# Optimization experiments

Measured on AMD Instinct MI355X. Metric: run time of the kernel, lower is better.

Reference implementation:

```python
import jax, jax.numpy as jnp
import numpy as np

INPUT_DIM = 28
HIDDEN = 256
N_LAYERS = 4
OUT_DIM = 21


def setup_inputs() -> dict:
    key = jax.random.key(0)
    ks = jax.random.split(key, 20)
    s = 1.0 / np.sqrt(HIDDEN)  # PyTorch LSTM init scale
    x = jax.random.normal(ks[0], (256, 512, INPUT_DIM), dtype=jnp.float32)
    W_ih0 = jax.random.uniform(ks[1], (4 * HIDDEN, INPUT_DIM), minval=-s, maxval=s, dtype=jnp.float32)
    W_ih_rest = jax.random.uniform(ks[2], (N_LAYERS - 1, 4 * HIDDEN, HIDDEN), minval=-s, maxval=s, dtype=jnp.float32)
    W_hh = jax.random.uniform(ks[3], (N_LAYERS, 4 * HIDDEN, HIDDEN), minval=-s, maxval=s, dtype=jnp.float32)
    b_ih = jax.random.uniform(ks[4], (N_LAYERS, 4 * HIDDEN), minval=-s, maxval=s, dtype=jnp.float32)
    b_hh = jax.random.uniform(ks[5], (N_LAYERS, 4 * HIDDEN), minval=-s, maxval=s, dtype=jnp.float32)
    W_out = jax.random.uniform(ks[6], (OUT_DIM, HIDDEN), minval=-s, maxval=s, dtype=jnp.float32)
    b_out = jax.random.uniform(ks[7], (OUT_DIM,), minval=-s, maxval=s, dtype=jnp.float32)
    return {"x": x, "W_ih0": W_ih0, "W_ih_rest": W_ih_rest, "W_hh": W_hh,
            "b_ih": b_ih, "b_hh": b_hh, "W_out": W_out, "b_out": b_out}


def _lstm_layer(x, W_ih, W_hh, b_ih, b_hh):
    # x: [B, T, D_in] -> [B, T, H]. PyTorch gate order: i, f, g, o.
    B, T, _ = x.shape
    H = W_hh.shape[1]
    # Precompute input projections for all timesteps: [T, B, 4H]
    xp = jnp.einsum('btd,gd->tbg', x, W_ih) + b_ih + b_hh

    def step(carry, xt):
        h, c = carry
        gates = xt + h @ W_hh.T  # [B, 4H]
        i, f, g, o = jnp.split(gates, 4, axis=-1)
        i = jax.nn.sigmoid(i)
        f = jax.nn.sigmoid(f)
        g = jnp.tanh(g)
        o = jax.nn.sigmoid(o)
        c = f * c + i * g
        h = o * jnp.tanh(c)
        return (h, c), h

    h0 = jnp.zeros((B, H), dtype=x.dtype)
    c0 = jnp.zeros((B, H), dtype=x.dtype)
    _, hs = jax.lax.scan(step, (h0, c0), xp)  # hs: [T, B, H]
    return jnp.transpose(hs, (1, 0, 2))  # [B, T, H]


def reference(x, W_ih0, W_ih_rest, W_hh, b_ih, b_hh, W_out, b_out):
    h = _lstm_layer(x, W_ih0, W_hh[0], b_ih[0], b_hh[0])
    for l in range(1, N_LAYERS):
        h = _lstm_layer(h, W_ih_rest[l - 1], W_hh[l], b_ih[l], b_hh[l])
    last = h[:, -1, :]  # [B, H]
    return jax.nn.sigmoid(last @ W_out.T + b_out)  # [B, OUT_DIM]
```

## Files before the change

kernel.cpp:

```cpp
#include <hip/hip_runtime.h>
#include <stdint.h>


#define B 256
#define T 512
#define H 256
#define DIN 28
#define NWG 256
#define OUTD 21

typedef __attribute__((ext_vector_type(8))) __bf16 bf16x8;
typedef __attribute__((ext_vector_type(4))) float f32x4;
typedef __attribute__((ext_vector_type(4))) unsigned short u16x4;
typedef unsigned long long u64;

#define WS_FLAGS 0ull
#define WS_HBUF  65536ull
#define WS_H3F   (WS_HBUF + 4ull*4*B*H*2)
#define WS_XBF   (WS_H3F + (u64)B*H*4)
#define WS_WIH0  (WS_XBF + (u64)B*T*32*2)
#define WS_WIHR  (WS_WIH0 + 1024ull*32*2)
#define WS_WHHR  (WS_WIHR + 3ull*1024*256*2)
#define WS_BIAS  (WS_WHHR + 4ull*1024*256*2)
#define WS_ZERO  WS_XBF

__device__ __forceinline__ unsigned short f2bf(float f) {
  unsigned u = __builtin_bit_cast(unsigned, f);
  u += 0x7fffu + ((u >> 16) & 1u);
  return (unsigned short)(u >> 16);
}
__device__ __forceinline__ float sigf(float x) { return 1.f / (1.f + __expf(-x)); }
__device__ __forceinline__ float tanhfast(float x) {
  float e = __expf(2.f * x);
  return 1.f - 2.f / (e + 1.f);
}
__device__ __forceinline__ bf16x8 ldb8(const void* p) { return *(const bf16x8*)p; }

__device__ __forceinline__ void stg_coh8(void* p, u64 v) {
  __hip_atomic_store((u64*)p, v, __ATOMIC_RELAXED, __HIP_MEMORY_SCOPE_AGENT);
}
__device__ __forceinline__ u64 ldq(const u64* p) {
  return __hip_atomic_load(p, __ATOMIC_RELAXED, __HIP_MEMORY_SCOPE_AGENT);
}
__device__ __forceinline__ unsigned ldflag(const unsigned* f) {
  return __hip_atomic_load(f, __ATOMIC_RELAXED, __HIP_MEMORY_SCOPE_AGENT);
}

__global__ void prep_x(const float* __restrict__ x, unsigned short* __restrict__ xbf) {
  int tot = B * T * 32;
  for (int idx = blockIdx.x * blockDim.x + threadIdx.x; idx < tot;
       idx += gridDim.x * blockDim.x) {
    int kk = idx & 31;
    int bt = idx >> 5;
    float v = (kk < DIN) ? x[(size_t)bt * DIN + kk] : 0.f;
    xbf[idx] = f2bf(v);
  }
}

__global__ void prep_w(const float* __restrict__ wih0, const float* __restrict__ wihrest,
                       const float* __restrict__ whh, const float* __restrict__ bih,
                       const float* __restrict__ bhh,
                       unsigned short* __restrict__ wih0r, unsigned short* __restrict__ wihr,
                       unsigned short* __restrict__ whhr, float* __restrict__ biasr) {
  const int R0 = 1024 * 32, R1 = 3 * 1024 * 256, R2 = 4 * 1024 * 256, R3 = 4 * 1024;
  int tot = R0 + R1 + R2 + R3;
  for (int idx = blockIdx.x * blockDim.x + threadIdx.x; idx < tot;
       idx += gridDim.x * blockDim.x) {
    if (idx < R0) {
      int k = idx & 31, np = idx >> 5, g = np & 3, j = np >> 2;
      wih0r[idx] = f2bf(k < DIN ? wih0[(size_t)(g * 256 + j) * DIN + k] : 0.f);
    } else if (idx < R0 + R1) {
      int i = idx - R0;
      int k = i & 255, r = i >> 8, np = r & 1023, l = r >> 10, g = np & 3, j = np >> 2;
      wihr[i] = f2bf(wihrest[((size_t)l * 1024 + g * 256 + j) * 256 + k]);
    } else if (idx < R0 + R1 + R2) {
      int i = idx - R0 - R1;
      int k = i & 255, r = i >> 8, np = r & 1023, l = r >> 10, g = np & 3, j = np >> 2;
      whhr[i] = f2bf(whh[((size_t)l * 1024 + g * 256 + j) * 256 + k]);
    } else {
      int i = idx - R0 - R1 - R2;
      int np = i & 1023, l = i >> 10, g = np & 3, j = np >> 2;
      biasr[i] = bih[l * 1024 + g * 256 + j] + bhh[l * 1024 + g * 256 + j];
    }
  }
}

__device__ __forceinline__ bf16x8 lds_frag(const unsigned char* base, int row, int kb) {
  return *(const bf16x8*)(base + row * 1024 + (kb ^ ((row & 15) << 4)));
}

__device__ __forceinline__ void mstep(const unsigned char* Ast, const unsigned char* Ws,
                                      int kb, int ar0, int ar1, int br0, int br1,
                                      f32x4& a00, f32x4& a01, f32x4& a10, f32x4& a11) {
  bf16x8 a0 = lds_frag(Ast, ar0, kb);
  bf16x8 a1 = lds_frag(Ast, ar1, kb);
  bf16x8 b0 = lds_frag(Ws, br0, kb);
  bf16x8 b1 = lds_frag(Ws, br1, kb);
  a00 = __builtin_amdgcn_mfma_f32_16x16x32_bf16(a0, b0, a00, 0, 0, 0);
  a01 = __builtin_amdgcn_mfma_f32_16x16x32_bf16(a0, b1, a01, 0, 0, 0);
  a10 = __builtin_amdgcn_mfma_f32_16x16x32_bf16(a1, b0, a10, 0, 0, 0);
  a11 = __builtin_amdgcn_mfma_f32_16x16x32_bf16(a1, b1, a11, 0, 0, 0);
}

__launch_bounds__(256, 1)
__global__ void lstm_main(const unsigned short* __restrict__ xbf,
                          const unsigned short* __restrict__ wih0r,
                          const unsigned short* __restrict__ wihr,
                          const unsigned short* __restrict__ whhr,
                          const float* __restrict__ biasr,
                          const float* __restrict__ Wout, const float* __restrict__ bout,
                          unsigned short* __restrict__ hbuf, float* __restrict__ h3f,
                          unsigned* __restrict__ flags, float* __restrict__ out) {
  __shared__ unsigned char Ws[64 * 1024];
  __shared__ unsigned char Ast[64 * 1024];
  __shared__ float gates[64 * 68];

  const int tid = threadIdx.x;
  const int lane = tid & 63;
  const int w = tid >> 6;
  const int wb = w >> 1, wn = w & 1;
  const int bid = blockIdx.x;
  const int layer = (bid & 7) >> 1;
  const int wgl = ((bid >> 3) << 1) | (bid & 1);
  const int b0g = wgl >> 4;
  const int b0 = b0g * 64;
  const int ntile = wgl & 15;
  const int n0 = ntile * 64;
  const int j0 = ntile * 16;
  const int mygrp = layer * 4 + b0g;

  const int ngr = (layer == 0) ? 36 : 64;
  for (int i = tid; i < 64 * ngr; i += 256) {
    int row = i / ngr, blk = i % ngr;
    uint4 v;
    if (layer == 0) {
      if (blk < 4) v = *(const uint4*)(wih0r + (size_t)(n0 + row) * 32 + blk * 8);
      else v = *(const uint4*)(whhr + (size_t)(n0 + row) * 256 + (blk - 4) * 8);
    } else {
      if (blk < 32)
        v = *(const uint4*)(wihr + ((size_t)(layer - 1) * 1024 + n0 + row) * 256 + blk * 8);
      else
        v = *(const uint4*)(whhr + ((size_t)layer * 1024 + n0 + row) * 256 + (blk - 32) * 8);
    }
    *(uint4*)(Ws + row * 1024 + ((blk * 16) ^ ((row & 15) << 4))) = v;
  }
  const float bv0 = biasr[layer * 1024 + n0 + wn * 32 + (lane & 15)];
  const float bv1 = biasr[layer * 1024 + n0 + wn * 32 + 16 + (lane & 15)];
  __syncthreads();

  const int arow0 = wb * 32 + (lane & 15);
  const int arow1 = arow0 + 16;
  const int akoff2 = (lane >> 4) * 16;
  const int brow0 = wn * 32 + (lane & 15);
  const int brow1 = brow0 + 16;

  const int stg_blk = tid & 63;
  const int stg_r0 = tid >> 6;

  f32x4 creg = {0.f, 0.f, 0.f, 0.f};

  for (int t = 0; t < T; ++t) {
    if (tid == 0) {
      const unsigned* frec = (t > 0) ? &flags[mygrp * 512 + (t - 1)] : nullptr;
      const unsigned* fprev = (layer > 0) ? &flags[(mygrp - 4) * 512 + t] : nullptr;
      const unsigned* fdown = (layer < 3 && t >= 4) ? &flags[(mygrp + 4) * 512 + (t - 4)] : nullptr;
      for (;;) {
        unsigned a = frec ? ldflag(frec) : 16u;
        unsigned b = fprev ? ldflag(fprev) : 16u;
        unsigned c = fdown ? ldflag(fdown) : 16u;
        if (a >= 16u && b >= 16u && c >= 16u) break;
        __builtin_amdgcn_s_sleep(1);
      }
    }
    __syncthreads();
    asm volatile("" ::: "memory");

    const unsigned short* hbR = hbuf + ((size_t)layer * 4 + ((t + 3) & 3)) * 65536;
    if (layer == 0) {
      u64 qa[16], qb[16];
#pragma unroll
      for (int it = 0; it < 16; ++it) {
        int row = b0 + stg_r0 + it * 4;
        if (stg_blk < 4) {
          bf16x8 v = ldb8(xbf + ((size_t)row * T + t) * 32 + stg_blk * 8);
          qa[it] = ((const u64*)&v)[0];
          qb[it] = ((const u64*)&v)[1];
        } else if (stg_blk < 36) {
          const u64* s = (const u64*)(hbR + (size_t)row * 256 + (stg_blk - 4) * 8);
          qa[it] = ldq(s);
          qb[it] = ldq(s + 1);
        }
      }
      __builtin_amdgcn_sched_barrier(0);
      if (stg_blk < 36) {
#pragma unroll
        for (int it = 0; it < 16; ++it) {
          int row = stg_r0 + it * 4;
          uint4 v;
          ((u64*)&v)[0] = qa[it];
          ((u64*)&v)[1] = qb[it];
          *(uint4*)(Ast + row * 1024 + ((stg_blk * 16) ^ ((row & 15) << 4))) = v;
        }
      }
    } else {
      const unsigned short* hbP = hbuf + ((size_t)(layer - 1) * 4 + (t & 3)) * 65536;
      const unsigned short* src = (stg_blk < 32) ? hbP + stg_blk * 8 : hbR + (stg_blk - 32) * 8;
      u64 qa[16], qb[16];
#pragma unroll
      for (int it = 0; it < 16; ++it) {
        int row = b0 + stg_r0 + it * 4;
        const u64* s = (const u64*)(src + (size_t)row * 256);
        qa[it] = ldq(s);
        qb[it] = ldq(s + 1);
      }
      __builtin_amdgcn_sched_barrier(0);
#pragma unroll
      for (int it = 0; it < 16; ++it) {
        int row = stg_r0 + it * 4;
        uint4 v;
        ((u64*)&v)[0] = qa[it];
        ((u64*)&v)[1] = qb[it];
        *(uint4*)(Ast + row * 1024 + ((stg_blk * 16) ^ ((row & 15) << 4))) = v;
      }
    }
    __syncthreads();

    f32x4 a00 = {bv0, bv0, bv0, bv0};
    f32x4 a01 = {bv1, bv1, bv1, bv1};
    f32x4 a10 = a00, a11 = a01;
    if (layer == 0) {
#pragma unroll
      for (int ki = 0; ki < 9; ++ki)
        mstep(Ast, Ws, ki * 64 + akoff2, arow0, arow1, brow0, brow1, a00, a01, a10, a11);
    } else {
#pragma unroll
      for (int ki = 0; ki < 16; ++ki)
        mstep(Ast, Ws, ki * 64 + akoff2, arow0, arow1, brow0, brow1, a00, a01, a10, a11);
    }

    {
      int c = lane & 15, Rg = lane >> 4;
      *(f32x4*)&gates[(wn * 32 + c) * 68 + wb * 32 + Rg * 4] = a00;
      *(f32x4*)&gates[(wn * 32 + 16 + c) * 68 + wb * 32 + Rg * 4] = a01;
      *(f32x4*)&gates[(wn * 32 + c) * 68 + wb * 32 + 16 + Rg * 4] = a10;
      *(f32x4*)&gates[(wn * 32 + 16 + c) * 68 + wb * 32 + 16 + Rg * 4] = a11;
    }
    __syncthreads();

    {
      int brel = tid & 63, jq = tid >> 6;
      int b = b0 + brel;
      int jb = j0 + jq * 4;
      f32x4 cnew;
      float hv[4];
#pragma unroll
      for (int i2 = 0; i2 < 4; ++i2) {
        int jr = jq * 4 + i2;
        float ip = gates[(4 * jr + 0) * 68 + brel];
        float fp = gates[(4 * jr + 1) * 68 + brel];
        float gp = gates[(4 * jr + 2) * 68 + brel];
        float op = gates[(4 * jr + 3) * 68 + brel];
        float ii = sigf(ip), ff = sigf(fp), gg = tanhfast(gp), oo = sigf(op);
        float cc = ff * creg[i2] + ii * gg;
        cnew[i2] = cc;
        hv[i2] = oo * tanhfast(cc);
      }
      creg = cnew;
      u16x4 h4 = {f2bf(hv[0]), f2bf(hv[1]), f2bf(hv[2]), f2bf(hv[3])};
      stg_coh8(hbuf + ((size_t)layer * 4 + (t & 3)) * 65536 + (size_t)b * H + jb,
               __builtin_bit_cast(u64, h4));
      if (layer == 3 && t == T - 1) {
        float2 p01 = make_float2(hv[0], hv[1]);
        float2 p23 = make_float2(hv[2], hv[3]);
        stg_coh8(h3f + (size_t)b * H + jb, __builtin_bit_cast(u64, p01));
        stg_coh8(h3f + (size_t)b * H + jb + 2, __builtin_bit_cast(u64, p23));
      }
    }
    asm volatile("s_waitcnt vmcnt(0)" ::: "memory");
    __syncthreads();
    if (tid == 0)
      __hip_atomic_fetch_add(&flags[mygrp * 512 + t], 1u, __ATOMIC_RELAXED,
                             __HIP_MEMORY_SCOPE_AGENT);
  }

  if (layer == 3) {
    if (tid == 0) {
      while (ldflag(&flags[mygrp * 512 + (T - 1)]) < 16u) __builtin_amdgcn_s_sleep(1);
    }
    __syncthreads();
    asm volatile("" ::: "memory");
    for (int i = tid; i < 4 * 128; i += 256) {
      int bi = i >> 7, jj = (i & 127) * 2;
      u64 q = ldq((const u64*)(h3f + (size_t)(b0 + ntile * 4 + bi) * H + jj));
      float2 hf = __builtin_bit_cast(float2, q);
      gates[bi * 260 + jj] = hf.x;
      gates[bi * 260 + jj + 1] = hf.y;
    }
    __syncthreads();
    if (tid < 4 * OUTD) {
      int o = tid % OUTD, bi = tid / OUTD;
      int b = b0 + ntile * 4 + bi;
      const float* wr = Wout + (size_t)o * H;
      const float* hr = &gates[bi * 260];
      float sum = bout[o];
#pragma unroll 8
      for (int j = 0; j < H; ++j) sum = fmaf(hr[j], wr[j], sum);
      out[b * OUTD + o] = sigf(sum);
    }
  }
}

extern "C" void kernel_launch(void* const* d_in, const int* in_sizes, int n_in,
                              void* d_out, int out_size, void* d_ws, size_t ws_size,
                              hipStream_t stream) {
  const float* x = (const float*)d_in[0];
  const float* Wih0 = (const float*)d_in[1];
  const float* WihRest = (const float*)d_in[2];
  const float* Whh = (const float*)d_in[3];
  const float* bih = (const float*)d_in[4];
  const float* bhh = (const float*)d_in[5];
  const float* Wout = (const float*)d_in[6];
  const float* bout = (const float*)d_in[7];
  float* out = (float*)d_out;
  char* ws = (char*)d_ws;

  unsigned* flags = (unsigned*)(ws + WS_FLAGS);
  unsigned short* hbuf = (unsigned short*)(ws + WS_HBUF);
  float* h3f = (float*)(ws + WS_H3F);
  unsigned short* xbf = (unsigned short*)(ws + WS_XBF);
  unsigned short* wih0r = (unsigned short*)(ws + WS_WIH0);
  unsigned short* wihr = (unsigned short*)(ws + WS_WIHR);
  unsigned short* whhr = (unsigned short*)(ws + WS_WHHR);
  float* biasr = (float*)(ws + WS_BIAS);

  hipMemsetAsync(ws, 0, (size_t)WS_ZERO, stream);
  prep_x<<<2048, 256, 0, stream>>>(x, xbf);
  prep_w<<<2048, 256, 0, stream>>>(Wih0, WihRest, Whh, bih, bhh, wih0r, wihr, whhr, biasr);
  lstm_main<<<NWG, 256, 0, stream>>>(xbf, wih0r, wihr, whhr, biasr, Wout, bout, hbuf,
                                     h3f, flags, out);
}
```

Before: 2.760 ms.

## Replace per-step flag counters with parity bits embedded in h data

Drops the per-timestep atomic flag counters, barrier and vmcnt wait. Each h value now carries a parity bit in the LSB of its first bf16, so consumer threads poll the data itself until every row shows the expected epoch. The h ring buffer grows from 4 to 8 slots, and backpressure becomes a sparse per-tile progress array checked every other step. The input-projection half of the K loop runs before waiting for the recurrent h, overlapping that matmul with the dependency wait. The risks are a one-bit precision loss in h, busy polling on data loads, and the subtle correctness of the epoch and backpressure logic.

```diff
diff --git a/kernel.cpp b/kernel.cpp
--- a/kernel.cpp
+++ b/kernel.cpp
@@ -14,36 +14,34 @@
 typedef __attribute__((ext_vector_type(4))) unsigned short u16x4;
 typedef unsigned long long u64;
 
-#define WS_FLAGS 0ull
-#define WS_HBUF  65536ull
-#define WS_H3F   (WS_HBUF + 4ull*4*B*H*2)
-#define WS_XBF   (WS_H3F + (u64)B*H*4)
+#define WS_PROG  0ull
+#define WS_HBUF  2048ull
+#define WS_XBF   (WS_HBUF + 4ull*8*B*H*2)
 #define WS_WIH0  (WS_XBF + (u64)B*T*32*2)
 #define WS_WIHR  (WS_WIH0 + 1024ull*32*2)
 #define WS_WHHR  (WS_WIHR + 3ull*1024*256*2)
 #define WS_BIAS  (WS_WHHR + 4ull*1024*256*2)
-#define WS_ZERO  WS_XBF
+#define WS_ZERO  WS_HBUF
 
 __device__ __forceinline__ unsigned short f2bf(float f) {
   unsigned u = __builtin_bit_cast(unsigned, f);
   u += 0x7fffu + ((u >> 16) & 1u);
   return (unsigned short)(u >> 16);
 }
+__device__ __forceinline__ float bf2f(unsigned short v) {
+  return __builtin_bit_cast(float, (unsigned)v << 16);
+}
 __device__ __forceinline__ float sigf(float x) { return 1.f / (1.f + __expf(-x)); }
 __device__ __forceinline__ float tanhfast(float x) {
   float e = __expf(2.f * x);
   return 1.f - 2.f / (e + 1.f);
 }
-__device__ __forceinline__ bf16x8 ldb8(const void* p) { return *(const bf16x8*)p; }
 
 __device__ __forceinline__ void stg_coh8(void* p, u64 v) {
   __hip_atomic_store((u64*)p, v, __ATOMIC_RELAXED, __HIP_MEMORY_SCOPE_AGENT);
 }
 __device__ __forceinline__ u64 ldq(const u64* p) {
   return __hip_atomic_load(p, __ATOMIC_RELAXED, __HIP_MEMORY_SCOPE_AGENT);
-}
-__device__ __forceinline__ unsigned ldflag(const unsigned* f) {
-  return __hip_atomic_load(f, __ATOMIC_RELAXED, __HIP_MEMORY_SCOPE_AGENT);
 }
 
 __global__ void prep_x(const float* __restrict__ x, unsigned short* __restrict__ xbf) {
@@ -55,6 +53,13 @@
     float v = (kk < DIN) ? x[(size_t)bt * DIN + kk] : 0.f;
     xbf[idx] = f2bf(v);
   }
+}
+
+__global__ void prep_fill(u64* __restrict__ hb) {
+  const size_t n = 4ull * 8 * B * H / 4;
+  for (size_t i = blockIdx.x * blockDim.x + threadIdx.x; i < n;
+       i += (size_t)gridDim.x * blockDim.x)
+    hb[i] = 0x0001000100010001ull;
 }
 
 __global__ void prep_w(const float* __restrict__ wih0, const float* __restrict__ wihrest,
@@ -109,10 +114,10 @@
                           const unsigned short* __restrict__ whhr,
                           const float* __restrict__ biasr,
                           const float* __restrict__ Wout, const float* __restrict__ bout,
-                          unsigned short* __restrict__ hbuf, float* __restrict__ h3f,
-                          unsigned* __restrict__ flags, float* __restrict__ out) {
+                          unsigned short* __restrict__ hbuf, unsigned* __restrict__ prog,
+                          float* __restrict__ out) {
   __shared__ unsigned char Ws[64 * 1024];
-  __shared__ unsigned char Ast[64 * 1024];
+  __shared__ unsigned char Ap[64 * 1024];
   __shared__ float gates[64 * 68];
 
   const int tid = threadIdx.x;
@@ -154,88 +159,139 @@
   const int brow0 = wn * 32 + (lane & 15);
   const int brow1 = brow0 + 16;
 
-  const int stg_blk = tid & 63;
-  const int stg_r0 = tid >> 6;
+  const int scol = tid & 31;
+  const int srow = tid >> 5;
+  const int xcol = tid & 3;
+  const int xrow = tid >> 2;
+
+  const int recbase = (layer == 0) ? 64 : 512;
 
   f32x4 creg = {0.f, 0.f, 0.f, 0.f};
+  u64 pA[16], rr[16], pr[8];
+
+  if (layer == 0) {
+    const u64* s = (const u64*)(xbf + ((size_t)(b0 + xrow) * T + 0) * 32 + xcol * 8);
+    pA[0] = s[0];
+    pA[1] = s[1];
+  } else {
+    const unsigned short* hbP = hbuf + ((size_t)(layer - 1) * 8 + 0) * 65536;
+#pragma unroll
+    for (int i = 0; i < 8; ++i) {
+      const u64* s = (const u64*)(hbP + (size_t)(b0 + srow + 8 * i) * 256 + scol * 8);
+      pA[2 * i] = ldq(s);
+      pA[2 * i + 1] = ldq(s + 1);
+    }
+  }
 
   for (int t = 0; t < T; ++t) {
-    if (tid == 0) {
-      const unsigned* frec = (t > 0) ? &flags[mygrp * 512 + (t - 1)] : nullptr;
-      const unsigned* fprev = (layer > 0) ? &flags[(mygrp - 4) * 512 + t] : nullptr;
-      const unsigned* fdown = (layer < 3 && t >= 4) ? &flags[(mygrp + 4) * 512 + (t - 4)] : nullptr;
+    const unsigned e_t = ((unsigned)t >> 3) & 1u;
+    const unsigned e_rec = ((((unsigned)t + 7) >> 3) & 1u) ^ 1u;
+    const bool bp = (layer < 3) && (t >= 8) && ((t & 1) == 0);
+
+    if (layer == 0) {
+      uint4 v;
+      ((u64*)&v)[0] = pA[0];
+      ((u64*)&v)[1] = pA[1];
+      *(uint4*)(Ap + xrow * 1024 + ((xcol * 16) ^ ((xrow & 15) << 4))) = v;
+    } else {
+      const unsigned short* hbP = hbuf + ((size_t)(layer - 1) * 8 + (t & 7)) * 65536;
       for (;;) {
-        unsigned a = frec ? ldflag(frec) : 16u;
-        unsigned b = fprev ? ldflag(fprev) : 16u;
-        unsigned c = fdown ? ldflag(fdown) : 16u;
-        if (a >= 16u && b >= 16u && c >= 16u) break;
+        u64 bad = 0;
+#pragma unroll
+        for (int i = 0; i < 16; ++i) bad |= (pA[i] ^ (u64)e_t) & 1ull;
+        if (!bad) break;
         __builtin_amdgcn_s_sleep(1);
-      }
-    }
-    __syncthreads();
-    asm volatile("" ::: "memory");
-
-    const unsigned short* hbR = hbuf + ((size_t)layer * 4 + ((t + 3) & 3)) * 65536;
-    if (layer == 0) {
-      u64 qa[16], qb[16];
-#pragma unroll
-      for (int it = 0; it < 16; ++it) {
-        int row = b0 + stg_r0 + it * 4;
-        if (stg_blk < 4) {
-          bf16x8 v = ldb8(xbf + ((size_t)row * T + t) * 32 + stg_blk * 8);
-          qa[it] = ((const u64*)&v)[0];
-          qb[it] = ((const u64*)&v)[1];
-        } else if (stg_blk < 36) {
-          const u64* s = (const u64*)(hbR + (size_t)row * 256 + (stg_blk - 4) * 8);
-          qa[it] = ldq(s);
-          qb[it] = ldq(s + 1);
+#pragma unroll
+        for (int i = 0; i < 8; ++i) {
+          const u64* s = (const u64*)(hbP + (size_t)(b0 + srow + 8 * i) * 256 + scol * 8);
+          pA[2 * i] = ldq(s);
+          pA[2 * i + 1] = ldq(s + 1);
         }
       }
-      __builtin_amdgcn_sched_barrier(0);
-      if (stg_blk < 36) {
-#pragma unroll
-        for (int it = 0; it < 16; ++it) {
-          int row = stg_r0 + it * 4;
-          uint4 v;
-          ((u64*)&v)[0] = qa[it];
-          ((u64*)&v)[1] = qb[it];
-          *(uint4*)(Ast + row * 1024 + ((stg_blk * 16) ^ ((row & 15) << 4))) = v;
-        }
-      }
-    } else {
-      const unsigned short* hbP = hbuf + ((size_t)(layer - 1) * 4 + (t & 3)) * 65536;
-      const unsigned short* src = (stg_blk < 32) ? hbP + stg_blk * 8 : hbR + (stg_blk - 32) * 8;
-      u64 qa[16], qb[16];
-#pragma unroll
-      for (int it = 0; it < 16; ++it) {
-        int row = b0 + stg_r0 + it * 4;
-        const u64* s = (const u64*)(src + (size_t)row * 256);
-        qa[it] = ldq(s);
-        qb[it] = ldq(s + 1);
-      }
-      __builtin_amdgcn_sched_barrier(0);
-#pragma unroll
-      for (int it = 0; it < 16; ++it) {
-        int row = stg_r0 + it * 4;
+#pragma unroll
+      for (int i = 0; i < 8; ++i) {
+        int row = srow + 8 * i;
         uint4 v;
-        ((u64*)&v)[0] = qa[it];
-        ((u64*)&v)[1] = qb[it];
-        *(uint4*)(Ast + row * 1024 + ((stg_blk * 16) ^ ((row & 15) << 4))) = v;
-      }
-    }
+        ((u64*)&v)[0] = pA[2 * i];
+        ((u64*)&v)[1] = pA[2 * i + 1];
+        *(uint4*)(Ap + row * 1024 + ((scol * 16) ^ ((row & 15) << 4))) = v;
+      }
+    }
+
+    const unsigned short* hbR = hbuf + ((size_t)layer * 8 + ((t - 1) & 7)) * 65536;
+#pragma unroll
+    for (int i = 0; i < 8; ++i) {
+      const u64* s = (const u64*)(hbR + (size_t)(b0 + srow + 8 * i) * 256 + scol * 8);
+      rr[2 * i] = ldq(s);
+      rr[2 * i + 1] = ldq(s + 1);
+    }
+    __builtin_amdgcn_sched_barrier(0);
     __syncthreads();
 
     f32x4 a00 = {bv0, bv0, bv0, bv0};
     f32x4 a01 = {bv1, bv1, bv1, bv1};
     f32x4 a10 = a00, a11 = a01;
     if (layer == 0) {
-#pragma unroll
-      for (int ki = 0; ki < 9; ++ki)
-        mstep(Ast, Ws, ki * 64 + akoff2, arow0, arow1, brow0, brow1, a00, a01, a10, a11);
+      mstep(Ap, Ws, akoff2, arow0, arow1, brow0, brow1, a00, a01, a10, a11);
     } else {
 #pragma unroll
-      for (int ki = 0; ki < 16; ++ki)
-        mstep(Ast, Ws, ki * 64 + akoff2, arow0, arow1, brow0, brow1, a00, a01, a10, a11);
+      for (int ki = 0; ki < 8; ++ki)
+        mstep(Ap, Ws, ki * 64 + akoff2, arow0, arow1, brow0, brow1, a00, a01, a10, a11);
+    }
+
+    for (;;) {
+      u64 bad = 0;
+#pragma unroll
+      for (int i = 0; i < 16; ++i) bad |= (rr[i] ^ (u64)e_rec) & 1ull;
+      if (!bad) break;
+      __builtin_amdgcn_s_sleep(1);
+#pragma unroll
+      for (int i = 0; i < 8; ++i) {
+        const u64* s = (const u64*)(hbR + (size_t)(b0 + srow + 8 * i) * 256 + scol * 8);
+        rr[2 * i] = ldq(s);
+        rr[2 * i + 1] = ldq(s + 1);
+      }
+    }
+#pragma unroll
+    for (int i = 0; i < 8; ++i) {
+      int row = srow + 8 * i;
+      uint4 v;
+      ((u64*)&v)[0] = rr[2 * i];
+      ((u64*)&v)[1] = rr[2 * i + 1];
+      *(uint4*)(Ap + row * 1024 + ((recbase + scol * 16) ^ ((row & 15) << 4))) = v;
+    }
+
+    if (bp) {
+      const u64* dp = (const u64*)(prog + (size_t)(mygrp + 4) * 16);
+#pragma unroll
+      for (int i = 0; i < 8; ++i) pr[i] = ldq(dp + i);
+    }
+    if (t + 1 < T) {
+      if (layer == 0) {
+        const u64* s = (const u64*)(xbf + ((size_t)(b0 + xrow) * T + (t + 1)) * 32 + xcol * 8);
+        pA[0] = s[0];
+        pA[1] = s[1];
+      } else {
+        const unsigned short* hbP2 = hbuf + ((size_t)(layer - 1) * 8 + ((t + 1) & 7)) * 65536;
+#pragma unroll
+        for (int i = 0; i < 8; ++i) {
+          const u64* s = (const u64*)(hbP2 + (size_t)(b0 + srow + 8 * i) * 256 + scol * 8);
+          pA[2 * i] = ldq(s);
+          pA[2 * i + 1] = ldq(s + 1);
+        }
+      }
+    }
+    __builtin_amdgcn_sched_barrier(0);
+    __syncthreads();
+
+    if (layer == 0) {
+#pragma unroll
+      for (int ki = 1; ki < 9; ++ki)
+        mstep(Ap, Ws, ki * 64 + akoff2, arow0, arow1, brow0, brow1, a00, a01, a10, a11);
+    } else {
+#pragma unroll
+      for (int ki = 8; ki < 16; ++ki)
+        mstep(Ap, Ws, ki * 64 + akoff2, arow0, arow1, brow0, brow1, a00, a01, a10, a11);
     }
 
     {
@@ -266,42 +322,57 @@
         hv[i2] = oo * tanhfast(cc);
       }
       creg = cnew;
-      u16x4 h4 = {f2bf(hv[0]), f2bf(hv[1]), f2bf(hv[2]), f2bf(hv[3])};
-      stg_coh8(hbuf + ((size_t)layer * 4 + (t & 3)) * 65536 + (size_t)b * H + jb,
+
+      if (bp) {
+        const u64* dp = (const u64*)(prog + (size_t)(mygrp + 4) * 16);
+        const unsigned need = (unsigned)(t - 6);
+        for (;;) {
+          unsigned mn = 0xFFFFFFFFu;
+#pragma unroll
+          for (int i = 0; i < 8; ++i) {
+            unsigned lo = (unsigned)pr[i], hi = (unsigned)(pr[i] >> 32);
+            mn = mn < lo ? mn : lo;
+            mn = mn < hi ? mn : hi;
+          }
+          if (mn >= need) break;
+          __builtin_amdgcn_s_sleep(1);
+#pragma unroll
+          for (int i = 0; i < 8; ++i) pr[i] = ldq(dp + i);
+        }
+      }
+
+      u16x4 h4 = {(unsigned short)((f2bf(hv[0]) & 0xFFFEu) | e_t), f2bf(hv[1]),
+                  f2bf(hv[2]), f2bf(hv[3])};
+      stg_coh8(hbuf + ((size_t)layer * 8 + (t & 7)) * 65536 + (size_t)b * H + jb,
                __builtin_bit_cast(u64, h4));
-      if (layer == 3 && t == T - 1) {
-        float2 p01 = make_float2(hv[0], hv[1]);
-        float2 p23 = make_float2(hv[2], hv[3]);
-        stg_coh8(h3f + (size_t)b * H + jb, __builtin_bit_cast(u64, p01));
-        stg_coh8(h3f + (size_t)b * H + jb + 2, __builtin_bit_cast(u64, p23));
-      }
-    }
-    asm volatile("s_waitcnt vmcnt(0)" ::: "memory");
-    __syncthreads();
-    if (tid == 0)
-      __hip_atomic_fetch_add(&flags[mygrp * 512 + t], 1u, __ATOMIC_RELAXED,
-                             __HIP_MEMORY_SCOPE_AGENT);
+    }
+    if (((t & 1) == 1) && tid == 0)
+      __hip_atomic_store(&prog[mygrp * 16 + ntile], (unsigned)(t + 1), __ATOMIC_RELAXED,
+                         __HIP_MEMORY_SCOPE_AGENT);
   }
 
   if (layer == 3) {
-    if (tid == 0) {
-      while (ldflag(&flags[mygrp * 512 + (T - 1)]) < 16u) __builtin_amdgcn_s_sleep(1);
-    }
-    __syncthreads();
-    asm volatile("" ::: "memory");
-    for (int i = tid; i < 4 * 128; i += 256) {
-      int bi = i >> 7, jj = (i & 127) * 2;
-      u64 q = ldq((const u64*)(h3f + (size_t)(b0 + ntile * 4 + bi) * H + jj));
-      float2 hf = __builtin_bit_cast(float2, q);
-      gates[bi * 260 + jj] = hf.x;
-      gates[bi * 260 + jj + 1] = hf.y;
-    }
+    const unsigned short* hp = hbuf + ((size_t)3 * 8 + ((T - 1) & 7)) * 65536;
+    const unsigned efin = (((unsigned)(T - 1)) >> 3) & 1u;
+    int bi = tid >> 6, gcol = tid & 63;
+    int brow = b0 + ntile * 4 + bi;
+    const u64* s = (const u64*)(hp + (size_t)brow * 256 + gcol * 4);
+    u64 v;
+    for (;;) {
+      v = ldq(s);
+      if (((unsigned)v & 1u) == efin) break;
+      __builtin_amdgcn_s_sleep(1);
+    }
+    gates[bi * 260 + gcol * 4 + 0] = bf2f((unsigned short)v);
+    gates[bi * 260 + gcol * 4 + 1] = bf2f((unsigned short)(v >> 16));
+    gates[bi * 260 + gcol * 4 + 2] = bf2f((unsigned short)(v >> 32));
+    gates[bi * 260 + gcol * 4 + 3] = bf2f((unsigned short)(v >> 48));
     __syncthreads();
     if (tid < 4 * OUTD) {
-      int o = tid % OUTD, bi = tid / OUTD;
-      int b = b0 + ntile * 4 + bi;
+      int o = tid % OUTD, bj = tid / OUTD;
+      int b = b0 + ntile * 4 + bj;
       const float* wr = Wout + (size_t)o * H;
-      const float* hr = &gates[bi * 260];
+      const float* hr = &gates[bj * 260];
       float sum = bout[o];
 #pragma unroll 8
       for (int j = 0; j < H; ++j) sum = fmaf(hr[j], wr[j], sum);
@@ -324,9 +395,8 @@
   float* out = (float*)d_out;
   char* ws = (char*)d_ws;
 
-  unsigned* flags = (unsigned*)(ws + WS_FLAGS);
+  unsigned* prog = (unsigned*)(ws + WS_PROG);
   unsigned short* hbuf = (unsigned short*)(ws + WS_HBUF);
-  float* h3f = (float*)(ws + WS_H3F);
   unsigned short* xbf = (unsigned short*)(ws + WS_XBF);
   unsigned short* wih0r = (unsigned short*)(ws + WS_WIH0);
   unsigned short* wihr = (unsigned short*)(ws + WS_WIHR);
@@ -334,8 +404,9 @@
   float* biasr = (float*)(ws + WS_BIAS);
 
   hipMemsetAsync(ws, 0, (size_t)WS_ZERO, stream);
+  prep_fill<<<1024, 256, 0, stream>>>((u64*)hbuf);
   prep_x<<<2048, 256, 0, stream>>>(x, xbf);
   prep_w<<<2048, 256, 0, stream>>>(Wih0, WihRest, Whh, bih, bhh, wih0r, wihr, whhr, biasr);
   lstm_main<<<NWG, 256, 0, stream>>>(xbf, wih0r, wihr, whhr, biasr, Wout, bout, hbuf,
-                                     h3f, flags, out);
-}
+                                     prog, out);
+}
```

Result: slower. 3.776 ms (+36.8%).

## Keep weights in registers and replace per-step counters with per-tile progress words

Applied to the files above, without the earlier changes.

Weight B-fragments now live in VGPRs (bA/bB arrays) instead of LDS, which removes the per-step LDS reads of weights and halves shared-memory use. The per-timestep flag counters (atomic fetch_add) are replaced by monotonic per-tile progress words that are read as a min over 16 entries, with cached up/down progress and spin-before-sleep polling. The staging layout is reorganized so each thread loads a contiguous 128-byte row chunk, and the t=0 recurrent matmul is skipped. The final fp32 h3 buffer is dropped and the output head reads the bf16 h instead, which slightly changes precision. The main risk is heavy register pressure from the 32 bf16x8 fragments.

```diff
diff --git a/kernel.cpp b/kernel.cpp
--- a/kernel.cpp
+++ b/kernel.cpp
@@ -14,36 +14,47 @@
 typedef __attribute__((ext_vector_type(4))) unsigned short u16x4;
 typedef unsigned long long u64;
 
-#define WS_FLAGS 0ull
-#define WS_HBUF  65536ull
-#define WS_H3F   (WS_HBUF + 4ull*4*B*H*2)
-#define WS_XBF   (WS_H3F + (u64)B*H*4)
+#define WS_SENT  0ull
+#define WS_HBUF  2048ull
+#define WS_XBF   (WS_HBUF + 4ull*4*B*H*2)
 #define WS_WIH0  (WS_XBF + (u64)B*T*32*2)
 #define WS_WIHR  (WS_WIH0 + 1024ull*32*2)
 #define WS_WHHR  (WS_WIHR + 3ull*1024*256*2)
 #define WS_BIAS  (WS_WHHR + 4ull*1024*256*2)
-#define WS_ZERO  WS_XBF
+#define WS_ZERO  2048ull
 
 __device__ __forceinline__ unsigned short f2bf(float f) {
   unsigned u = __builtin_bit_cast(unsigned, f);
   u += 0x7fffu + ((u >> 16) & 1u);
   return (unsigned short)(u >> 16);
 }
+__device__ __forceinline__ float bf2f(unsigned short v) {
+  return __builtin_bit_cast(float, (unsigned)v << 16);
+}
 __device__ __forceinline__ float sigf(float x) { return 1.f / (1.f + __expf(-x)); }
 __device__ __forceinline__ float tanhfast(float x) {
   float e = __expf(2.f * x);
   return 1.f - 2.f / (e + 1.f);
 }
-__device__ __forceinline__ bf16x8 ldb8(const void* p) { return *(const bf16x8*)p; }
-
-__device__ __forceinline__ void stg_coh8(void* p, u64 v) {
-  __hip_atomic_store((u64*)p, v, __ATOMIC_RELAXED, __HIP_MEMORY_SCOPE_AGENT);
-}
 __device__ __forceinline__ u64 ldq(const u64* p) {
   return __hip_atomic_load(p, __ATOMIC_RELAXED, __HIP_MEMORY_SCOPE_AGENT);
 }
-__device__ __forceinline__ unsigned ldflag(const unsigned* f) {
-  return __hip_atomic_load(f, __ATOMIC_RELAXED, __HIP_MEMORY_SCOPE_AGENT);
+__device__ __forceinline__ void stq(void* p, u64 v) {
+  __hip_atomic_store((u64*)p, v, __ATOMIC_RELAXED, __HIP_MEMORY_SCOPE_AGENT);
+}
+__device__ __forceinline__ void stw_agent(unsigned* p, unsigned v) {
+  __hip_atomic_store(p, v, __ATOMIC_RELAXED, __HIP_MEMORY_SCOPE_AGENT);
+}
+__device__ __forceinline__ unsigned umin2(unsigned a, unsigned b) { return a < b ? a : b; }
+__device__ __forceinline__ unsigned min16_agent(const unsigned* p) {
+  unsigned m = 0xFFFFFFFFu;
+  const u64* q = (const u64*)p;
+#pragma unroll
+  for (int i = 0; i < 8; ++i) {
+    u64 v = ldq(q + i);
+    m = umin2(m, umin2((unsigned)v, (unsigned)(v >> 32)));
+  }
+  return m;
 }
 
 __global__ void prep_x(const float* __restrict__ x, unsigned short* __restrict__ xbf) {
@@ -85,17 +96,11 @@
   }
 }
 
-__device__ __forceinline__ bf16x8 lds_frag(const unsigned char* base, int row, int kb) {
-  return *(const bf16x8*)(base + row * 1024 + (kb ^ ((row & 15) << 4)));
-}
-
-__device__ __forceinline__ void mstep(const unsigned char* Ast, const unsigned char* Ws,
-                                      int kb, int ar0, int ar1, int br0, int br1,
-                                      f32x4& a00, f32x4& a01, f32x4& a10, f32x4& a11) {
-  bf16x8 a0 = lds_frag(Ast, ar0, kb);
-  bf16x8 a1 = lds_frag(Ast, ar1, kb);
-  bf16x8 b0 = lds_frag(Ws, br0, kb);
-  bf16x8 b1 = lds_frag(Ws, br1, kb);
+__device__ __forceinline__ void mstep2(const unsigned char* Ap, int kb, int ar0, int ar1,
+                                       bf16x8 b0, bf16x8 b1, f32x4& a00, f32x4& a01,
+                                       f32x4& a10, f32x4& a11) {
+  bf16x8 a0 = *(const bf16x8*)(Ap + ar0 * 1024 + (kb ^ ((ar0 & 15) << 4)));
+  bf16x8 a1 = *(const bf16x8*)(Ap + ar1 * 1024 + (kb ^ ((ar1 & 15) << 4)));
   a00 = __builtin_amdgcn_mfma_f32_16x16x32_bf16(a0, b0, a00, 0, 0, 0);
   a01 = __builtin_amdgcn_mfma_f32_16x16x32_bf16(a0, b1, a01, 0, 0, 0);
   a10 = __builtin_amdgcn_mfma_f32_16x16x32_bf16(a1, b0, a10, 0, 0, 0);
@@ -109,10 +114,9 @@
                           const unsigned short* __restrict__ whhr,
                           const float* __restrict__ biasr,
                           const float* __restrict__ Wout, const float* __restrict__ bout,
-                          unsigned short* __restrict__ hbuf, float* __restrict__ h3f,
-                          unsigned* __restrict__ flags, float* __restrict__ out) {
-  __shared__ unsigned char Ws[64 * 1024];
-  __shared__ unsigned char Ast[64 * 1024];
+                          unsigned short* __restrict__ hbuf, unsigned* __restrict__ sent,
+                          float* __restrict__ out) {
+  __shared__ unsigned char Ap[64 * 1024];
   __shared__ float gates[64 * 68];
 
   const int tid = threadIdx.x;
@@ -129,98 +133,112 @@
   const int j0 = ntile * 16;
   const int mygrp = layer * 4 + b0g;
 
-  const int ngr = (layer == 0) ? 36 : 64;
-  for (int i = tid; i < 64 * ngr; i += 256) {
-    int row = i / ngr, blk = i % ngr;
-    uint4 v;
-    if (layer == 0) {
-      if (blk < 4) v = *(const uint4*)(wih0r + (size_t)(n0 + row) * 32 + blk * 8);
-      else v = *(const uint4*)(whhr + (size_t)(n0 + row) * 256 + (blk - 4) * 8);
-    } else {
-      if (blk < 32)
-        v = *(const uint4*)(wihr + ((size_t)(layer - 1) * 1024 + n0 + row) * 256 + blk * 8);
-      else
-        v = *(const uint4*)(whhr + ((size_t)layer * 1024 + n0 + row) * 256 + (blk - 32) * 8);
-    }
-    *(uint4*)(Ws + row * 1024 + ((blk * 16) ^ ((row & 15) << 4))) = v;
+  unsigned* sent_own = sent + mygrp * 16;
+  const unsigned* sent_up = (layer > 0) ? sent + (mygrp - 4) * 16 : sent_own;
+  const unsigned* sent_dn = (layer < 3) ? sent + (mygrp + 4) * 16 : sent_own;
+
+  const int brow0 = wn * 32 + (lane & 15);
+  const int brow1 = brow0 + 16;
+  const int koff8 = (lane >> 4) * 8;
+  const int akoff2 = (lane >> 4) * 16;
+  bf16x8 bA[16], bB[16];
+  if (layer == 0) {
+    bA[0] = *(const bf16x8*)(wih0r + (size_t)(n0 + brow0) * 32 + koff8);
+    bB[0] = *(const bf16x8*)(wih0r + (size_t)(n0 + brow1) * 32 + koff8);
+#pragma unroll
+    for (int kk = 0; kk < 8; ++kk) {
+      bA[1 + kk] = *(const bf16x8*)(whhr + (size_t)(n0 + brow0) * 256 + kk * 32 + koff8);
+      bB[1 + kk] = *(const bf16x8*)(whhr + (size_t)(n0 + brow1) * 256 + kk * 32 + koff8);
+    }
+  } else {
+#pragma unroll
+    for (int kk = 0; kk < 8; ++kk) {
+      bA[kk] = *(const bf16x8*)(wihr + ((size_t)(layer - 1) * 1024 + n0 + brow0) * 256 +
+                                kk * 32 + koff8);
+      bB[kk] = *(const bf16x8*)(wihr + ((size_t)(layer - 1) * 1024 + n0 + brow1) * 256 +
+                                kk * 32 + koff8);
+      bA[8 + kk] = *(const bf16x8*)(whhr + ((size_t)layer * 1024 + n0 + brow0) * 256 +
+                                    kk * 32 + koff8);
+      bB[8 + kk] = *(const bf16x8*)(whhr + ((size_t)layer * 1024 + n0 + brow1) * 256 +
+                                    kk * 32 + koff8);
+    }
   }
   const float bv0 = biasr[layer * 1024 + n0 + wn * 32 + (lane & 15)];
   const float bv1 = biasr[layer * 1024 + n0 + wn * 32 + 16 + (lane & 15)];
-  __syncthreads();
 
   const int arow0 = wb * 32 + (lane & 15);
   const int arow1 = arow0 + 16;
-  const int akoff2 = (lane >> 4) * 16;
-  const int brow0 = wn * 32 + (lane & 15);
-  const int brow1 = brow0 + 16;
-
-  const int stg_blk = tid & 63;
-  const int stg_r0 = tid >> 6;
+  const int strow = tid >> 2;
+  const int stchunk = tid & 3;
+  const int srs = (strow & 15) << 4;
+  const int recoff = (layer == 0) ? 64 : 512;
 
   f32x4 creg = {0.f, 0.f, 0.f, 0.f};
+  unsigned cache_up = 0, cache_dn = 0;
 
   for (int t = 0; t < T; ++t) {
     if (tid == 0) {
-      const unsigned* frec = (t > 0) ? &flags[mygrp * 512 + (t - 1)] : nullptr;
-      const unsigned* fprev = (layer > 0) ? &flags[(mygrp - 4) * 512 + t] : nullptr;
-      const unsigned* fdown = (layer < 3 && t >= 4) ? &flags[(mygrp + 4) * 512 + (t - 4)] : nullptr;
-      for (;;) {
-        unsigned a = frec ? ldflag(frec) : 16u;
-        unsigned b = fprev ? ldflag(fprev) : 16u;
-        unsigned c = fdown ? ldflag(fdown) : 16u;
-        if (a >= 16u && b >= 16u && c >= 16u) break;
-        __builtin_amdgcn_s_sleep(1);
+      int it = 0;
+      if (t > 0) {
+        while (min16_agent(sent_own) < (unsigned)t) {
+          if (++it > 32) __builtin_amdgcn_s_sleep(1);
+        }
+      }
+      if (layer > 0 && cache_up < (unsigned)(t + 1)) {
+        while ((cache_up = min16_agent(sent_up)) < (unsigned)(t + 1)) {
+          if (++it > 32) __builtin_amdgcn_s_sleep(1);
+        }
+      }
+      if (layer < 3 && t >= 4 && cache_dn < (unsigned)(t - 3)) {
+        while ((cache_dn = min16_agent(sent_dn)) < (unsigned)(t - 3)) {
+          if (++it > 32) __builtin_amdgcn_s_sleep(1);
+        }
       }
     }
     __syncthreads();
     asm volatile("" ::: "memory");
 
-    const unsigned short* hbR = hbuf + ((size_t)layer * 4 + ((t + 3) & 3)) * 65536;
+    u64 rv[16], pv[16];
+    uint4 xg;
+    const unsigned short* hbR = hbuf + ((size_t)layer * 4 + ((t - 1) & 3)) * 65536;
+    if (t > 0) {
+      const u64* rp = (const u64*)(hbR + (size_t)(b0 + strow) * 256 + stchunk * 64);
+#pragma unroll
+      for (int i = 0; i < 16; ++i) rv[i] = ldq(rp + i);
+    }
     if (layer == 0) {
-      u64 qa[16], qb[16];
-#pragma unroll
-      for (int it = 0; it < 16; ++it) {
-        int row = b0 + stg_r0 + it * 4;
-        if (stg_blk < 4) {
-          bf16x8 v = ldb8(xbf + ((size_t)row * T + t) * 32 + stg_blk * 8);
-          qa[it] = ((const u64*)&v)[0];
-          qb[it] = ((const u64*)&v)[1];
-        } else if (stg_blk < 36) {
-          const u64* s = (const u64*)(hbR + (size_t)row * 256 + (stg_blk - 4) * 8);
-          qa[it] = ldq(s);
-          qb[it] = ldq(s + 1);
-        }
-      }
-      __builtin_amdgcn_sched_barrier(0);
-      if (stg_blk < 36) {
-#pragma unroll
-        for (int it = 0; it < 16; ++it) {
-          int row = stg_r0 + it * 4;
+      xg = *(const uint4*)(xbf + ((size_t)(b0 + strow) * T + t) * 32 + stchunk * 8);
+    } else {
+      const u64* pp = (const u64*)(hbuf + ((size_t)(layer - 1) * 4 + (t & 3)) * 65536 +
+                                   (size_t)(b0 + strow) * 256 + stchunk * 64);
+#pragma unroll
+      for (int i = 0; i < 16; ++i) pv[i] = ldq(pp + i);
+    }
+    __builtin_amdgcn_sched_barrier(0);
+
+    {
+      unsigned char* wbase = Ap + strow * 1024;
+      if (t > 0) {
+        int rb = recoff + stchunk * 128;
+#pragma unroll
+        for (int i = 0; i < 8; ++i) {
           uint4 v;
-          ((u64*)&v)[0] = qa[it];
-          ((u64*)&v)[1] = qb[it];
-          *(uint4*)(Ast + row * 1024 + ((stg_blk * 16) ^ ((row & 15) << 4))) = v;
-        }
-      }
-    } else {
-      const unsigned short* hbP = hbuf + ((size_t)(layer - 1) * 4 + (t & 3)) * 65536;
-      const unsigned short* src = (stg_blk < 32) ? hbP + stg_blk * 8 : hbR + (stg_blk - 32) * 8;
-      u64 qa[16], qb[16];
-#pragma unroll
-      for (int it = 0; it < 16; ++it) {
-        int row = b0 + stg_r0 + it * 4;
-        const u64* s = (const u64*)(src + (size_t)row * 256);
-        qa[it] = ldq(s);
-        qb[it] = ldq(s + 1);
-      }
-      __builtin_amdgcn_sched_barrier(0);
-#pragma unroll
-      for (int it = 0; it < 16; ++it) {
-        int row = stg_r0 + it * 4;
-        uint4 v;
-        ((u64*)&v)[0] = qa[it];
-        ((u64*)&v)[1] = qb[it];
-        *(uint4*)(Ast + row * 1024 + ((stg_blk * 16) ^ ((row & 15) << 4))) = v;
+          ((u64*)&v)[0] = rv[2 * i];
+          ((u64*)&v)[1] = rv[2 * i + 1];
+          *(uint4*)(wbase + ((rb + i * 16) ^ srs)) = v;
+        }
+      }
+      if (layer == 0) {
+        *(uint4*)(wbase + ((stchunk * 16) ^ srs)) = xg;
+      } else {
+        int pb = stchunk * 128;
+#pragma unroll
+        for (int i = 0; i < 8; ++i) {
+          uint4 v;
+          ((u64*)&v)[0] = pv[2 * i];
+          ((u64*)&v)[1] = pv[2 * i + 1];
+          *(uint4*)(wbase + ((pb + i * 16) ^ srs)) = v;
+        }
       }
     }
     __syncthreads();
@@ -229,13 +247,23 @@
     f32x4 a01 = {bv1, bv1, bv1, bv1};
     f32x4 a10 = a00, a11 = a01;
     if (layer == 0) {
-#pragma unroll
-      for (int ki = 0; ki < 9; ++ki)
-        mstep(Ast, Ws, ki * 64 + akoff2, arow0, arow1, brow0, brow1, a00, a01, a10, a11);
+      mstep2(Ap, akoff2, arow0, arow1, bA[0], bB[0], a00, a01, a10, a11);
+      if (t > 0) {
+#pragma unroll
+        for (int kk = 0; kk < 8; ++kk)
+          mstep2(Ap, 64 + kk * 64 + akoff2, arow0, arow1, bA[1 + kk], bB[1 + kk],
+                 a00, a01, a10, a11);
+      }
     } else {
 #pragma unroll
-      for (int ki = 0; ki < 16; ++ki)
-        mstep(Ast, Ws, ki * 64 + akoff2, arow0, arow1, brow0, brow1, a00, a01, a10, a11);
+      for (int kk = 0; kk < 8; ++kk)
+        mstep2(Ap, kk * 64 + akoff2, arow0, arow1, bA[kk], bB[kk], a00, a01, a10, a11);
+      if (t > 0) {
+#pragma unroll
+        for (int kk = 0; kk < 8; ++kk)
+          mstep2(Ap, 512 + kk * 64 + akoff2, arow0, arow1, bA[8 + kk], bB[8 + kk],
+                 a00, a01, a10, a11);
+      }
     }
 
     {
@@ -267,41 +295,39 @@
       }
       creg = cnew;
       u16x4 h4 = {f2bf(hv[0]), f2bf(hv[1]), f2bf(hv[2]), f2bf(hv[3])};
-      stg_coh8(hbuf + ((size_t)layer * 4 + (t & 3)) * 65536 + (size_t)b * H + jb,
-               __builtin_bit_cast(u64, h4));
-      if (layer == 3 && t == T - 1) {
-        float2 p01 = make_float2(hv[0], hv[1]);
-        float2 p23 = make_float2(hv[2], hv[3]);
-        stg_coh8(h3f + (size_t)b * H + jb, __builtin_bit_cast(u64, p01));
-        stg_coh8(h3f + (size_t)b * H + jb + 2, __builtin_bit_cast(u64, p23));
-      }
+      stq(hbuf + ((size_t)layer * 4 + (t & 3)) * 65536 + (size_t)b * H + jb,
+          __builtin_bit_cast(u64, h4));
     }
     asm volatile("s_waitcnt vmcnt(0)" ::: "memory");
     __syncthreads();
-    if (tid == 0)
-      __hip_atomic_fetch_add(&flags[mygrp * 512 + t], 1u, __ATOMIC_RELAXED,
-                             __HIP_MEMORY_SCOPE_AGENT);
+    if (tid == 0) stw_agent(sent_own + ntile, (unsigned)(t + 1));
   }
 
   if (layer == 3) {
     if (tid == 0) {
-      while (ldflag(&flags[mygrp * 512 + (T - 1)]) < 16u) __builtin_amdgcn_s_sleep(1);
+      int it = 0;
+      while (min16_agent(sent_own) < (unsigned)T) {
+        if (++it > 32) __builtin_amdgcn_s_sleep(1);
+      }
     }
     __syncthreads();
     asm volatile("" ::: "memory");
-    for (int i = tid; i < 4 * 128; i += 256) {
-      int bi = i >> 7, jj = (i & 127) * 2;
-      u64 q = ldq((const u64*)(h3f + (size_t)(b0 + ntile * 4 + bi) * H + jj));
-      float2 hf = __builtin_bit_cast(float2, q);
-      gates[bi * 260 + jj] = hf.x;
-      gates[bi * 260 + jj + 1] = hf.y;
+    {
+      int bi = tid >> 6, gcol = tid & 63;
+      int brow2 = b0 + ntile * 4 + bi;
+      const unsigned short* hp = hbuf + ((size_t)3 * 4 + ((T - 1) & 3)) * 65536;
+      u64 v = ldq((const u64*)(hp + (size_t)brow2 * 256 + gcol * 4));
+      gates[bi * 260 + gcol * 4 + 0] = bf2f((unsigned short)v);
+      gates[bi * 260 + gcol * 4 + 1] = bf2f((unsigned short)(v >> 16));
+      gates[bi * 260 + gcol * 4 + 2] = bf2f((unsigned short)(v >> 32));
+      gates[bi * 260 + gcol * 4 + 3] = bf2f((unsigned short)(v >> 48));
     }
     __syncthreads();
     if (tid < 4 * OUTD) {
-      int o = tid % OUTD, bi = tid / OUTD;
-      int b = b0 + ntile * 4 + bi;
+      int o = tid % OUTD, bj = tid / OUTD;
+      int b = b0 + ntile * 4 + bj;
       const float* wr = Wout + (size_t)o * H;
-      const float* hr = &gates[bi * 260];
+      const float* hr = &gates[bj * 260];
       float sum = bout[o];
 #pragma unroll 8
       for (int j = 0; j < H; ++j) sum = fmaf(hr[j], wr[j], sum);
@@ -324,9 +350,8 @@
   float* out = (float*)d_out;
   char* ws = (char*)d_ws;
 
-  unsigned* flags = (unsigned*)(ws + WS_FLAGS);
+  unsigned* sent = (unsigned*)(ws + WS_SENT);
   unsigned short* hbuf = (unsigned short*)(ws + WS_HBUF);
-  float* h3f = (float*)(ws + WS_H3F);
   unsigned short* xbf = (unsigned short*)(ws + WS_XBF);
   unsigned short* wih0r = (unsigned short*)(ws + WS_WIH0);
   unsigned short* wihr = (unsigned short*)(ws + WS_WIHR);
@@ -337,5 +362,5 @@
   prep_x<<<2048, 256, 0, stream>>>(x, xbf);
   prep_w<<<2048, 256, 0, stream>>>(Wih0, WihRest, Whh, bih, bhh, wih0r, wihr, whhr, biasr);
   lstm_main<<<NWG, 256, 0, stream>>>(xbf, wih0r, wihr, whhr, biasr, Wout, bout, hbuf,
-                                     h3f, flags, out);
-}
+                                     sent, out);
+}
```

New measurement: 7.478 ms. +170.9%, slower.
